# Performance work log

Measured on AMD Instinct MI355X. Metric: run time of the kernel, lower is better.

Reference implementation:

```python
import jax, jax.numpy as jnp
import numpy as np

EPS = 1e-5


def _lstm_agg(x, nbr_idx, Wih, Whh, bih, bhh):
    # x: [N, D] node feats; nbr_idx: [N, K]; LSTM hidden size == D (DGL lstm aggregator)
    seq = x[nbr_idx]                     # [N, K, D] irregular gather
    N, K, D = seq.shape
    seq_t = jnp.swapaxes(seq, 0, 1)      # [K, N, D] time-major for scan

    def step(carry, xt):
        h, c = carry
        z = xt @ Wih.T + bih + h @ Whh.T + bhh   # [N, 4D]; torch gate order i,f,g,o
        i, f, g, o = jnp.split(z, 4, axis=-1)
        i = jax.nn.sigmoid(i)
        f = jax.nn.sigmoid(f)
        g = jnp.tanh(g)
        o = jax.nn.sigmoid(o)
        c = f * c + i * g
        h = o * jnp.tanh(c)
        return (h, c), None

    zero = jnp.zeros((N, D), seq.dtype)
    (h, _), _ = jax.lax.scan(step, (zero, zero), seq_t)
    return h                             # final hidden state = neighbor aggregate


def _sage_layer(x, nbr_idx, Wih, Whh, bih, bhh, Wself, bself, Wneigh):
    h_neigh = _lstm_agg(x, nbr_idx, Wih, Whh, bih, bhh)
    return x @ Wself.T + bself + h_neigh @ Wneigh.T


def _bn(x, gamma, beta):
    # BatchNorm1d in training mode: batch statistics over the node axis
    mu = jnp.mean(x, axis=0)
    var = jnp.var(x, axis=0)
    return (x - mu) * jax.lax.rsqrt(var + EPS) * gamma + beta


def setup_inputs() -> dict:
    key = jax.random.key(0)
    N, K, D_IN, D_H = 100000, 16, 128, 128
    ks = jax.random.split(key, 20)
    s = 0.05
    inp = {
        "in_feat": jax.random.normal(ks[0], (N, D_IN), jnp.float32),
        "nbr_idx": jax.random.randint(ks[1], (N, K), 0, N, jnp.int32),
        # layer 1 (in_feats=128 -> h_feats=128), LSTM hidden = in_feats
        "Wih1": jax.random.normal(ks[2], (4 * D_IN, D_IN), jnp.float32) * s,
        "Whh1": jax.random.normal(ks[3], (4 * D_IN, D_IN), jnp.float32) * s,
        "bih1": jnp.zeros((4 * D_IN,), jnp.float32),
        "bhh1": jnp.zeros((4 * D_IN,), jnp.float32),
        "Wself1": jax.random.normal(ks[4], (D_H, D_IN), jnp.float32) * s,
        "bself1": jnp.zeros((D_H,), jnp.float32),
        "Wneigh1": jax.random.normal(ks[5], (D_H, D_IN), jnp.float32) * s,
        "gamma1": jnp.ones((D_H,), jnp.float32),
        "beta1": jnp.zeros((D_H,), jnp.float32),
        # layer 2 (h_feats=128 -> h_feats=128)
        "Wih2": jax.random.normal(ks[6], (4 * D_H, D_H), jnp.float32) * s,
        "Whh2": jax.random.normal(ks[7], (4 * D_H, D_H), jnp.float32) * s,
        "bih2": jnp.zeros((4 * D_H,), jnp.float32),
        "bhh2": jnp.zeros((4 * D_H,), jnp.float32),
        "Wself2": jax.random.normal(ks[8], (D_H, D_H), jnp.float32) * s,
        "bself2": jnp.zeros((D_H,), jnp.float32),
        "Wneigh2": jax.random.normal(ks[9], (D_H, D_H), jnp.float32) * s,
        "gamma2": jnp.ones((D_H,), jnp.float32),
        "beta2": jnp.zeros((D_H,), jnp.float32),
    }
    return inp


def reference(in_feat, nbr_idx,
              Wih1, Whh1, bih1, bhh1, Wself1, bself1, Wneigh1, gamma1, beta1,
              Wih2, Whh2, bih2, bhh2, Wself2, bself2, Wneigh2, gamma2, beta2):
    h = _sage_layer(in_feat, nbr_idx, Wih1, Whh1, bih1, bhh1, Wself1, bself1, Wneigh1)
    h = jax.nn.relu(_bn(h, gamma1, beta1))
    h = _sage_layer(h, nbr_idx, Wih2, Whh2, bih2, bhh2, Wself2, bself2, Wneigh2)
    h = _bn(h, gamma2, beta2)
    return h
```

## Files before the change

### kernel.cpp

```cpp
#include <hip/hip_runtime.h>

typedef unsigned short u16;
typedef unsigned int u32;
typedef unsigned long long u64;
typedef __attribute__((ext_vector_type(8))) short short8;
typedef __attribute__((ext_vector_type(4))) float float4_t;
typedef __attribute__((ext_vector_type(2))) u32 u32x2;

__device__ __forceinline__ u16 f2bf(float f) {
    union { float f; u32 u; } x; x.f = f;
    u32 r = x.u + 0x7FFFu + ((x.u >> 16) & 1u);
    return (u16)(r >> 16);
}
__device__ __forceinline__ float bitsf(u32 u) {
    union { u32 u; float f; } x; x.u = u; return x.f;
}
__device__ __forceinline__ u32 pk2bf(float hi, float lo) {
    union { float f; u32 u; } a, b; a.f = hi; b.f = lo;
    return __builtin_amdgcn_perm(a.u + 0x8000u, b.u + 0x8000u, 0x07060302u);
}
#define LOG2E 1.44269504088896340736f
__device__ __forceinline__ float tanh_(float x) {
    float t = __builtin_amdgcn_exp2f(2.f * LOG2E * x);
    return 1.f - 2.f * __builtin_amdgcn_rcpf(1.f + t);
}

__device__ __forceinline__ float4_t mfma16(short8 a, short8 b, float4_t c) {
    return __builtin_amdgcn_mfma_f32_16x16x32_bf16(a, b, c, 0, 0, 0);
}

#define LDS_BARRIER() asm volatile("s_waitcnt lgkmcnt(0)\n\ts_barrier" ::: "memory")

__device__ __forceinline__ short8 ldfrag(const u16* p) { return *(const short8*)p; }
__device__ __forceinline__ short8 ldfrag(const float* p) {
    float4_t a = *(const float4_t*)p;
    float4_t b = *(const float4_t*)(p + 4);
    short8 r;
#pragma unroll
    for (int j = 0; j < 4; ++j) { r[j] = (short)f2bf(a[j]); r[4 + j] = (short)f2bf(b[j]); }
    return r;
}
__device__ __forceinline__ short8 ldfrag_scaled(const float* p, float s) {
    float4_t a = *(const float4_t*)p;
    float4_t b = *(const float4_t*)(p + 4);
    short8 r;
#pragma unroll
    for (int j = 0; j < 4; ++j) { r[j] = (short)f2bf(a[j] * s); r[4 + j] = (short)f2bf(b[j] * s); }
    return r;
}

template<typename AT>
__global__ __launch_bounds__(256) void gemm_ih(
    const AT* __restrict__ A, const float* __restrict__ W,
    const float* __restrict__ b1, const float* __restrict__ b2,
    u16* __restrict__ C, float* __restrict__ stats, int M)
{
    if (blockIdx.x == 0 && blockIdx.y == 0) stats[threadIdx.x] = 0.f;
    const int P = 512;
    const int lane = threadIdx.x & 63;
    const int w    = threadIdx.x >> 6;
    const int l15  = lane & 15;
    const int quad = lane >> 4;
    const int rowbase = blockIdx.x * 64;
    const int colbase = blockIdx.y * 128 + w * 32;

    short8 af[4][4];
#pragma unroll
    for (int mb = 0; mb < 4; ++mb) {
        int row = rowbase + mb * 16 + l15;
        if (row >= M) row = M - 1;
        const AT* ap = A + (size_t)row * 128 + quad * 8;
#pragma unroll
        for (int kb = 0; kb < 4; ++kb) af[mb][kb] = ldfrag(ap + kb * 32);
    }
    short8 bfr[2][4];
#pragma unroll
    for (int nb = 0; nb < 2; ++nb) {
        int col = colbase + nb * 16 + l15;
        const float* wp = W + (size_t)col * 128 + quad * 8;
#pragma unroll
        for (int kb = 0; kb < 4; ++kb) bfr[nb][kb] = ldfrag(wp + kb * 32);
    }
    const float4_t z4 = {0.f, 0.f, 0.f, 0.f};
    float bias[2], scl[2];
#pragma unroll
    for (int nb = 0; nb < 2; ++nb) {
        int col = colbase + nb * 16 + l15;
        bias[nb] = b1[col] + b2[col];
        scl[nb] = (col >= 256 && col < 384) ? (2.f * LOG2E) : (-LOG2E);
    }
#pragma unroll
    for (int mb = 0; mb < 4; ++mb)
#pragma unroll
        for (int nb = 0; nb < 2; ++nb) {
            float4_t a = z4;
#pragma unroll
            for (int kb = 0; kb < 4; ++kb) a = mfma16(af[mb][kb], bfr[nb][kb], a);
#pragma unroll
            for (int r = 0; r < 4; ++r) {
                int row = rowbase + mb * 16 + quad * 4 + r;
                int col = colbase + nb * 16 + l15;
                if (row < M) C[(size_t)row * P + col] = f2bf((a[r] + bias[nb]) * scl[nb]);
            }
        }
}

template<typename T>
__device__ __forceinline__ void accum_gemm(
    const T* __restrict__ A, const float* __restrict__ W,
    float4_t (&acc)[4][2], int M, int rowbase, int colbase, int l15, int quad)
{
    short8 af[4][4];
#pragma unroll
    for (int mb = 0; mb < 4; ++mb) {
        int row = rowbase + mb * 16 + l15;
        if (row >= M) row = M - 1;
        const T* ap = A + (size_t)row * 128 + quad * 8;
#pragma unroll
        for (int kb = 0; kb < 4; ++kb) af[mb][kb] = ldfrag(ap + kb * 32);
    }
    short8 bfr[2][4];
#pragma unroll
    for (int nb = 0; nb < 2; ++nb) {
        int col = colbase + nb * 16 + l15;
        const float* wp = W + (size_t)col * 128 + quad * 8;
#pragma unroll
        for (int kb = 0; kb < 4; ++kb) bfr[nb][kb] = ldfrag(wp + kb * 32);
    }
#pragma unroll
    for (int mb = 0; mb < 4; ++mb)
#pragma unroll
        for (int nb = 0; nb < 2; ++nb)
#pragma unroll
            for (int kb = 0; kb < 4; ++kb)
                acc[mb][nb] = mfma16(af[mb][kb], bfr[nb][kb], acc[mb][nb]);
}

template<typename AT2>
__global__ __launch_bounds__(256) void gemm_out(
    const u16* __restrict__ A1, const float* __restrict__ W1,
    const AT2* __restrict__ A2, const float* __restrict__ W2,
    const float* __restrict__ bias, float* __restrict__ C,
    float* __restrict__ stats, int M)
{
    const int P = 128;
    const int lane = threadIdx.x & 63;
    const int w    = threadIdx.x >> 6;
    const int l15  = lane & 15;
    const int quad = lane >> 4;
    const int rowbase = blockIdx.x * 64;
    const int colbase = w * 32;

    float4_t acc[4][2];
    const float4_t z4 = {0.f, 0.f, 0.f, 0.f};
#pragma unroll
    for (int mb = 0; mb < 4; ++mb)
#pragma unroll
        for (int nb = 0; nb < 2; ++nb) acc[mb][nb] = z4;

    accum_gemm(A1, W1, acc, M, rowbase, colbase, l15, quad);
    accum_gemm(A2, W2, acc, M, rowbase, colbase, l15, quad);

    float s[2] = {0.f, 0.f}, sq[2] = {0.f, 0.f};
#pragma unroll
    for (int nb = 0; nb < 2; ++nb) {
        int col = colbase + nb * 16 + l15;
        float bb = bias[col];
#pragma unroll
        for (int mb = 0; mb < 4; ++mb)
#pragma unroll
            for (int r = 0; r < 4; ++r) {
                int row = rowbase + mb * 16 + quad * 4 + r;
                if (row < M) {
                    float v = acc[mb][nb][r] + bb;
                    C[(size_t)row * P + col] = v;
                    s[nb] += v; sq[nb] += v * v;
                }
            }
    }
#pragma unroll
    for (int nb = 0; nb < 2; ++nb) {
        float t1 = s[nb], t2 = sq[nb];
        t1 += __shfl_xor(t1, 16); t1 += __shfl_xor(t1, 32);
        t2 += __shfl_xor(t2, 16); t2 += __shfl_xor(t2, 32);
        int col = colbase + nb * 16 + l15;
        if (quad == 0) atomicAdd(&stats[col], t1);
        if (quad == 1) atomicAdd(&stats[P + col], t2);
    }
}

__global__ __launch_bounds__(512, 2) void lstm_kernel(
    const u16* __restrict__ Xih,
    const int* __restrict__ nbr,
    const float* __restrict__ Whh,
    u16* __restrict__ Hout,
    int N)
{
    __shared__ u16 hbuf[2][64][128];
    __shared__ int nbrs[16][72];
    const int tid  = threadIdx.x;
    const int lane = tid & 63;
    const int w    = tid >> 6;
    const int l15  = lane & 15;
    const int quad = lane >> 4;
    const int base = blockIdx.x * 64;

    short8 whA[4][4];
#pragma unroll
    for (int g = 0; g < 4; ++g) {
        int row = 128 * g + 16 * w + l15;
        float s = (g == 2) ? (2.f * LOG2E) : (-LOG2E);
        const float* wp = Whh + (size_t)row * 128 + quad * 8;
#pragma unroll
        for (int kb = 0; kb < 4; ++kb) whA[g][kb] = ldfrag_scaled(wp + kb * 32, s);
    }
    u32* hz = (u32*)&hbuf[0][0][0];
    for (int i = tid; i < 2 * 64 * 128 / 2; i += 512) hz[i] = 0u;
    for (int i = tid; i < 64 * 16; i += 512) {
        int node = base + (i >> 4);
        if (node >= N) node = N - 1;
        nbrs[i & 15][i >> 4] = nbr[(size_t)node * 16 + (i & 15)];
    }
    __syncthreads();

    const int xoff = 16 * w + 4 * quad;

    u32x2 xfu[4][4];
#pragma unroll
    for (int nb = 0; nb < 4; ++nb) {
        int node = nbrs[0][l15 + 16 * nb];
        const u16* xp = Xih + (size_t)node * 512 + xoff;
#pragma unroll
        for (int g = 0; g < 4; ++g) xfu[nb][g] = *(const u32x2*)(xp + 128 * g);
    }

    const float4_t z4 = {0.f, 0.f, 0.f, 0.f};
    float4_t c[4];
#pragma unroll
    for (int nb = 0; nb < 4; ++nb) c[nb] = z4;

    for (int t = 0; t < 16; ++t) {
        const int p = t & 1;
#pragma unroll
        for (int nb = 0; nb < 4; ++nb) {
            const int row = l15 + 16 * nb;
            float4_t z[4];
#pragma unroll
            for (int g = 0; g < 4; ++g) {
                u32 w0 = xfu[nb][g][0], w1 = xfu[nb][g][1];
                z[g][0] = bitsf(w0 << 16); z[g][1] = bitsf(w0 & 0xFFFF0000u);
                z[g][2] = bitsf(w1 << 16); z[g][3] = bitsf(w1 & 0xFFFF0000u);
            }
            if (t < 15) {
                int node = nbrs[t + 1][row];
                const u16* xp = Xih + (size_t)node * 512 + xoff;
#pragma unroll
                for (int g = 0; g < 4; ++g) xfu[nb][g] = *(const u32x2*)(xp + 128 * g);
            }
            const char* hrow = (const char*)&hbuf[p][row][0];
            __builtin_amdgcn_s_setprio(1);
#pragma unroll
            for (int kb = 0; kb < 4; ++kb) {
                int ch = (quad + 4 * kb) ^ (row & 7);
                short8 hb = *(const short8*)(hrow + (ch << 4));
#pragma unroll
                for (int g = 0; g < 4; ++g)
                    z[g] = mfma16(whA[g][kb], hb, z[g]);
            }
            __builtin_amdgcn_s_setprio(0);
            float4_t hv;
#pragma unroll
            for (int r = 0; r < 4; ++r) {
                float i_ = __builtin_amdgcn_rcpf(1.f + __builtin_amdgcn_exp2f(z[0][r]));
                float f_ = __builtin_amdgcn_rcpf(1.f + __builtin_amdgcn_exp2f(z[1][r]));
                float g_ = 1.f - 2.f * __builtin_amdgcn_rcpf(1.f + __builtin_amdgcn_exp2f(z[2][r]));
                float o_ = __builtin_amdgcn_rcpf(1.f + __builtin_amdgcn_exp2f(z[3][r]));
                float cc = f_ * c[nb][r] + i_ * g_;
                c[nb][r] = cc;
                hv[r] = o_ * tanh_(cc);
            }
            u64 pkd = ((u64)pk2bf(hv[3], hv[2]) << 32) | pk2bf(hv[1], hv[0]);
            if (t < 15) {
                int ch = (2 * w + (quad >> 1)) ^ (row & 7);
                int sw = (ch << 4) | ((quad & 1) << 3);
                *(u64*)((char*)&hbuf[1 - p][row][0] + sw) = pkd;
            } else {
                int grow = base + row;
                if (grow < N)
                    *(u64*)(Hout + (size_t)grow * 128 + xoff) = pkd;
            }
        }
        if (t < 15) LDS_BARRIER();
    }
}

__global__ void bn_prep(float* stats, const float* __restrict__ gamma,
                        const float* __restrict__ beta, float invN)
{
    int cidx = threadIdx.x;
    float s = stats[cidx], sq = stats[128 + cidx];
    float mu = s * invN;
    float var = sq * invN - mu * mu;
    float sc = gamma[cidx] * rsqrtf(var + 1e-5f);
    stats[256 + cidx] = sc;
    stats[384 + cidx] = beta[cidx] - mu * sc;
}

template<typename OT>
__global__ __launch_bounds__(256) void bn_apply(
    const float* __restrict__ X, const float* __restrict__ stats,
    OT* __restrict__ Y, int M, int relu)
{
    int gid = blockIdx.x * 256 + threadIdx.x;
    int row = gid >> 4;
    int cs  = (gid & 15) * 8;
    if (row >= M) return;
    float4_t a = *(const float4_t*)(X + (size_t)row * 128 + cs);
    float4_t b = *(const float4_t*)(X + (size_t)row * 128 + cs + 4);
    float v[8];
#pragma unroll
    for (int j = 0; j < 8; ++j) {
        float x = (j < 4) ? a[j] : b[j - 4];
        float t = x * stats[256 + cs + j] + stats[384 + cs + j];
        v[j] = relu ? fmaxf(t, 0.f) : t;
    }
    if constexpr (sizeof(OT) == 2) {
        short8 ov;
#pragma unroll
        for (int j = 0; j < 8; ++j) ov[j] = (short)f2bf(v[j]);
        *(short8*)((u16*)Y + (size_t)row * 128 + cs) = ov;
    } else {
        float4_t o1, o2;
#pragma unroll
        for (int j = 0; j < 4; ++j) { o1[j] = v[j]; o2[j] = v[4 + j]; }
        *(float4_t*)((float*)Y + (size_t)row * 128 + cs) = o1;
        *(float4_t*)((float*)Y + (size_t)row * 128 + cs + 4) = o2;
    }
}

extern "C" void kernel_launch(void* const* d_in, const int* in_sizes, int n_in,
                              void* d_out, int out_size, void* d_ws, size_t ws_size,
                              hipStream_t stream)
{
    const float* in_feat = (const float*)d_in[0];
    const int*   nbr     = (const int*)d_in[1];
    const float* Wih1 = (const float*)d_in[2];
    const float* Whh1 = (const float*)d_in[3];
    const float* bih1 = (const float*)d_in[4];
    const float* bhh1 = (const float*)d_in[5];
    const float* Wself1  = (const float*)d_in[6];
    const float* bself1  = (const float*)d_in[7];
    const float* Wneigh1 = (const float*)d_in[8];
    const float* gamma1  = (const float*)d_in[9];
    const float* beta1   = (const float*)d_in[10];
    const float* Wih2 = (const float*)d_in[11];
    const float* Whh2 = (const float*)d_in[12];
    const float* bih2 = (const float*)d_in[13];
    const float* bhh2 = (const float*)d_in[14];
    const float* Wself2  = (const float*)d_in[15];
    const float* bself2  = (const float*)d_in[16];
    const float* Wneigh2 = (const float*)d_in[17];
    const float* gamma2  = (const float*)d_in[18];
    const float* beta2   = (const float*)d_in[19];

    const int N = in_sizes[0] / 128;

    char* ws = (char*)d_ws;
    u16*   Xih   = (u16*)ws;
    float* Pbuf  = (float*)ws;
    u16*   hn    = (u16*)(ws + (size_t)N * 1024);
    float* stats = (float*)(ws + (size_t)N * 1024 + (size_t)N * 256);
    u16*   hcur  = (u16*)d_out;

    const int nblk = (N + 63) / 64;
    const float invN = 1.0f / (float)N;
    const int bnblk = (N * 16 + 255) / 256;

    gemm_ih<float><<<dim3(nblk, 4), dim3(256), 0, stream>>>(in_feat, Wih1, bih1, bhh1, Xih, stats, N);
    lstm_kernel<<<dim3(nblk), dim3(512), 0, stream>>>(Xih, nbr, Whh1, hn, N);
    gemm_out<float><<<dim3(nblk, 1), dim3(256), 0, stream>>>(hn, Wneigh1, in_feat, Wself1,
                                                             bself1, Pbuf, stats, N);
    bn_prep<<<dim3(1), dim3(128), 0, stream>>>(stats, gamma1, beta1, invN);
    bn_apply<u16><<<dim3(bnblk), dim3(256), 0, stream>>>(Pbuf, stats, hcur, N, 1);

    gemm_ih<u16><<<dim3(nblk, 4), dim3(256), 0, stream>>>(hcur, Wih2, bih2, bhh2, Xih, stats, N);
    lstm_kernel<<<dim3(nblk), dim3(512), 0, stream>>>(Xih, nbr, Whh2, hn, N);
    gemm_out<u16><<<dim3(nblk, 1), dim3(256), 0, stream>>>(hn, Wneigh2, hcur, Wself2,
                                                           bself2, Pbuf, stats, N);
    bn_prep<<<dim3(1), dim3(128), 0, stream>>>(stats, gamma2, beta2, invN);
    bn_apply<float><<<dim3(bnblk), dim3(256), 0, stream>>>(Pbuf, stats, (float*)d_out, N, 0);
}
```

Before: 1.538 ms.

## Restructure LSTM kernel so each wave owns nodes and keeps Whh in LDS

New measurement: 5.234 ms. 3.4x slower.

```diff
diff --git a/kernel.cpp b/kernel.cpp
--- a/kernel.cpp
+++ b/kernel.cpp
@@ -6,6 +6,7 @@
 typedef __attribute__((ext_vector_type(8))) short short8;
 typedef __attribute__((ext_vector_type(4))) float float4_t;
 typedef __attribute__((ext_vector_type(2))) u32 u32x2;
+typedef __attribute__((ext_vector_type(4))) u32 u32x4;
 
 __device__ __forceinline__ u16 f2bf(float f) {
     union { float f; u32 u; } x; x.f = f;
@@ -28,8 +29,6 @@
 __device__ __forceinline__ float4_t mfma16(short8 a, short8 b, float4_t c) {
     return __builtin_amdgcn_mfma_f32_16x16x32_bf16(a, b, c, 0, 0, 0);
 }
-
-#define LDS_BARRIER() asm volatile("s_waitcnt lgkmcnt(0)\n\ts_barrier" ::: "memory")
 
 __device__ __forceinline__ short8 ldfrag(const u16* p) { return *(const short8*)p; }
 __device__ __forceinline__ short8 ldfrag(const float* p) {
@@ -38,14 +37,6 @@
     short8 r;
 #pragma unroll
     for (int j = 0; j < 4; ++j) { r[j] = (short)f2bf(a[j]); r[4 + j] = (short)f2bf(b[j]); }
-    return r;
-}
-__device__ __forceinline__ short8 ldfrag_scaled(const float* p, float s) {
-    float4_t a = *(const float4_t*)p;
-    float4_t b = *(const float4_t*)(p + 4);
-    short8 r;
-#pragma unroll
-    for (int j = 0; j < 4; ++j) { r[j] = (short)f2bf(a[j] * s); r[4 + j] = (short)f2bf(b[j] * s); }
     return r;
 }
 
@@ -189,108 +180,138 @@
     }
 }
 
-__global__ __launch_bounds__(512, 2) void lstm_kernel(
+__global__ __launch_bounds__(512) void lstm_kernel(
     const u16* __restrict__ Xih,
     const int* __restrict__ nbr,
     const float* __restrict__ Whh,
     u16* __restrict__ Hout,
     int N)
 {
-    __shared__ u16 hbuf[2][64][128];
-    __shared__ int nbrs[16][72];
+    __shared__ u16 whs[512 * 128];
+    __shared__ u32 scr[8][32][16];
     const int tid  = threadIdx.x;
     const int lane = tid & 63;
     const int w    = tid >> 6;
     const int l15  = lane & 15;
     const int quad = lane >> 4;
-    const int base = blockIdx.x * 64;
-
-    short8 whA[4][4];
-#pragma unroll
-    for (int g = 0; g < 4; ++g) {
-        int row = 128 * g + 16 * w + l15;
-        float s = (g == 2) ? (2.f * LOG2E) : (-LOG2E);
-        const float* wp = Whh + (size_t)row * 128 + quad * 8;
-#pragma unroll
-        for (int kb = 0; kb < 4; ++kb) whA[g][kb] = ldfrag_scaled(wp + kb * 32, s);
-    }
-    u32* hz = (u32*)&hbuf[0][0][0];
-    for (int i = tid; i < 2 * 64 * 128 / 2; i += 512) hz[i] = 0u;
-    for (int i = tid; i < 64 * 16; i += 512) {
-        int node = base + (i >> 4);
-        if (node >= N) node = N - 1;
-        nbrs[i & 15][i >> 4] = nbr[(size_t)node * 16 + (i & 15)];
+    const int base = blockIdx.x * 256;
+
+    for (int i = tid; i < 512 * 16; i += 512) {
+        const int R = i >> 4, cch = i & 15;
+        const float s = ((R >> 7) == 2) ? (2.f * LOG2E) : (-LOG2E);
+        const float* wp = Whh + (size_t)R * 128 + cch * 8;
+        float4_t a = *(const float4_t*)wp;
+        float4_t b = *(const float4_t*)(wp + 4);
+        u32x4 pk;
+        pk[0] = ((u32)f2bf(a[1] * s) << 16) | f2bf(a[0] * s);
+        pk[1] = ((u32)f2bf(a[3] * s) << 16) | f2bf(a[2] * s);
+        pk[2] = ((u32)f2bf(b[1] * s) << 16) | f2bf(b[0] * s);
+        pk[3] = ((u32)f2bf(b[3] * s) << 16) | f2bf(b[2] * s);
+        *(u32x4*)&whs[R * 128 + ((cch ^ (R & 15)) << 3)] = pk;
     }
     __syncthreads();
 
-    const int xoff = 16 * w + 4 * quad;
-
-    u32x2 xfu[4][4];
-#pragma unroll
-    for (int nb = 0; nb < 4; ++nb) {
-        int node = nbrs[0][l15 + 16 * nb];
-        const u16* xp = Xih + (size_t)node * 512 + xoff;
-#pragma unroll
-        for (int g = 0; g < 4; ++g) xfu[nb][g] = *(const u32x2*)(xp + 128 * g);
-    }
+    const int own0s = base + w * 32 + l15;
+    const int own1s = own0s + 16;
+    const int own0 = own0s < N ? own0s : N - 1;
+    const int own1 = own1s < N ? own1s : N - 1;
+
+    int xcur0 = nbr[(size_t)own0 * 16];
+    int xcur1 = nbr[(size_t)own1 * 16];
 
     const float4_t z4 = {0.f, 0.f, 0.f, 0.f};
-    float4_t c[4];
-#pragma unroll
-    for (int nb = 0; nb < 4; ++nb) c[nb] = z4;
+    float4_t c[8][2];
+#pragma unroll
+    for (int dc = 0; dc < 8; ++dc) { c[dc][0] = z4; c[dc][1] = z4; }
+    const short8 zs8 = {0, 0, 0, 0, 0, 0, 0, 0};
+    short8 hfA[2][4];
+#pragma unroll
+    for (int n = 0; n < 2; ++n)
+#pragma unroll
+        for (int kb = 0; kb < 4; ++kb) hfA[n][kb] = zs8;
 
     for (int t = 0; t < 16; ++t) {
-        const int p = t & 1;
-#pragma unroll
-        for (int nb = 0; nb < 4; ++nb) {
-            const int row = l15 + 16 * nb;
-            float4_t z[4];
-#pragma unroll
-            for (int g = 0; g < 4; ++g) {
-                u32 w0 = xfu[nb][g][0], w1 = xfu[nb][g][1];
-                z[g][0] = bitsf(w0 << 16); z[g][1] = bitsf(w0 & 0xFFFF0000u);
-                z[g][2] = bitsf(w1 << 16); z[g][3] = bitsf(w1 & 0xFFFF0000u);
+        int xn0 = 0, xn1 = 0;
+        if (t < 15) {
+            xn0 = nbr[(size_t)own0 * 16 + t + 1];
+            xn1 = nbr[(size_t)own1 * 16 + t + 1];
+        }
+        const u16* bp0 = Xih + (size_t)xcur0 * 512 + 4 * quad;
+        const u16* bp1 = Xih + (size_t)xcur1 * 512 + 4 * quad;
+
+        u32x2 gb[2][2][4];
+#pragma unroll
+        for (int g = 0; g < 4; ++g) {
+            gb[0][0][g] = *(const u32x2*)(bp0 + 128 * g);
+            gb[0][1][g] = *(const u32x2*)(bp1 + 128 * g);
+        }
+        short8 hfB[2][4];
+#pragma unroll
+        for (int dc = 0; dc < 8; ++dc) {
+            const int par = dc & 1;
+            if (dc < 7) {
+#pragma unroll
+                for (int g = 0; g < 4; ++g) {
+                    gb[par ^ 1][0][g] = *(const u32x2*)(bp0 + 128 * g + 16 * (dc + 1));
+                    gb[par ^ 1][1][g] = *(const u32x2*)(bp1 + 128 * g + 16 * (dc + 1));
+                }
             }
-            if (t < 15) {
-                int node = nbrs[t + 1][row];
-                const u16* xp = Xih + (size_t)node * 512 + xoff;
-#pragma unroll
-                for (int g = 0; g < 4; ++g) xfu[nb][g] = *(const u32x2*)(xp + 128 * g);
+            float4_t z[4][2];
+#pragma unroll
+            for (int g = 0; g < 4; ++g)
+#pragma unroll
+                for (int n = 0; n < 2; ++n) {
+                    u32 w0 = gb[par][n][g][0], w1 = gb[par][n][g][1];
+                    z[g][n][0] = bitsf(w0 << 16); z[g][n][1] = bitsf(w0 & 0xFFFF0000u);
+                    z[g][n][2] = bitsf(w1 << 16); z[g][n][3] = bitsf(w1 & 0xFFFF0000u);
+                }
+#pragma unroll
+            for (int kb = 0; kb < 4; ++kb)
+#pragma unroll
+                for (int g = 0; g < 4; ++g) {
+                    const short8 whf = *(const short8*)&whs[
+                        (128 * g + 16 * dc + l15) * 128 +
+                        ((((kb << 2) | quad) ^ l15) << 3)];
+                    z[g][0] = mfma16(whf, hfA[0][kb], z[g][0]);
+                    z[g][1] = mfma16(whf, hfA[1][kb], z[g][1]);
+                }
+#pragma unroll
+            for (int n = 0; n < 2; ++n) {
+                float4_t hv;
+#pragma unroll
+                for (int r = 0; r < 4; ++r) {
+                    float i_ = __builtin_amdgcn_rcpf(1.f + __builtin_amdgcn_exp2f(z[0][n][r]));
+                    float f_ = __builtin_amdgcn_rcpf(1.f + __builtin_amdgcn_exp2f(z[1][n][r]));
+                    float g_ = 1.f - 2.f * __builtin_amdgcn_rcpf(1.f + __builtin_amdgcn_exp2f(z[2][n][r]));
+                    float o_ = __builtin_amdgcn_rcpf(1.f + __builtin_amdgcn_exp2f(z[3][n][r]));
+                    float cc = f_ * c[dc][n][r] + i_ * g_;
+                    c[dc][n][r] = cc;
+                    hv[r] = o_ * tanh_(cc);
+                }
+                u32x2 pr;
+                pr[0] = pk2bf(hv[1], hv[0]);
+                pr[1] = pk2bf(hv[3], hv[2]);
+                if (t < 15) {
+                    *(u32x2*)&scr[w][n * 16 + l15][8 * par + 2 * quad] = pr;
+                } else {
+                    const int own = n ? own1s : own0s;
+                    if (own < N)
+                        *(u32x2*)(Hout + (size_t)own * 128 + 16 * dc + 4 * quad) = pr;
+                }
             }
-            const char* hrow = (const char*)&hbuf[p][row][0];
-            __builtin_amdgcn_s_setprio(1);
-#pragma unroll
-            for (int kb = 0; kb < 4; ++kb) {
-                int ch = (quad + 4 * kb) ^ (row & 7);
-                short8 hb = *(const short8*)(hrow + (ch << 4));
-#pragma unroll
-                for (int g = 0; g < 4; ++g)
-                    z[g] = mfma16(whA[g][kb], hb, z[g]);
-            }
-            __builtin_amdgcn_s_setprio(0);
-            float4_t hv;
-#pragma unroll
-            for (int r = 0; r < 4; ++r) {
-                float i_ = __builtin_amdgcn_rcpf(1.f + __builtin_amdgcn_exp2f(z[0][r]));
-                float f_ = __builtin_amdgcn_rcpf(1.f + __builtin_amdgcn_exp2f(z[1][r]));
-                float g_ = 1.f - 2.f * __builtin_amdgcn_rcpf(1.f + __builtin_amdgcn_exp2f(z[2][r]));
-                float o_ = __builtin_amdgcn_rcpf(1.f + __builtin_amdgcn_exp2f(z[3][r]));
-                float cc = f_ * c[nb][r] + i_ * g_;
-                c[nb][r] = cc;
-                hv[r] = o_ * tanh_(cc);
-            }
-            u64 pkd = ((u64)pk2bf(hv[3], hv[2]) << 32) | pk2bf(hv[1], hv[0]);
-            if (t < 15) {
-                int ch = (2 * w + (quad >> 1)) ^ (row & 7);
-                int sw = (ch << 4) | ((quad & 1) << 3);
-                *(u64*)((char*)&hbuf[1 - p][row][0] + sw) = pkd;
-            } else {
-                int grow = base + row;
-                if (grow < N)
-                    *(u64*)(Hout + (size_t)grow * 128 + xoff) = pkd;
+            if (par && t < 15) {
+                const int kb = dc >> 1;
+                hfB[0][kb] = *(const short8*)&scr[w][l15][4 * quad];
+                hfB[1][kb] = *(const short8*)&scr[w][16 + l15][4 * quad];
             }
         }
-        if (t < 15) LDS_BARRIER();
+        if (t < 15) {
+#pragma unroll
+            for (int n = 0; n < 2; ++n)
+#pragma unroll
+                for (int kb = 0; kb < 4; ++kb) hfA[n][kb] = hfB[n][kb];
+            xcur0 = xn0; xcur1 = xn1;
+        }
     }
 }
 
@@ -373,18 +394,19 @@
     u16*   hcur  = (u16*)d_out;
 
     const int nblk = (N + 63) / 64;
+    const int lblk = (N + 255) / 256;
     const float invN = 1.0f / (float)N;
     const int bnblk = (N * 16 + 255) / 256;
 
     gemm_ih<float><<<dim3(nblk, 4), dim3(256), 0, stream>>>(in_feat, Wih1, bih1, bhh1, Xih, stats, N);
-    lstm_kernel<<<dim3(nblk), dim3(512), 0, stream>>>(Xih, nbr, Whh1, hn, N);
+    lstm_kernel<<<dim3(lblk), dim3(512), 0, stream>>>(Xih, nbr, Whh1, hn, N);
     gemm_out<float><<<dim3(nblk, 1), dim3(256), 0, stream>>>(hn, Wneigh1, in_feat, Wself1,
                                                              bself1, Pbuf, stats, N);
     bn_prep<<<dim3(1), dim3(128), 0, stream>>>(stats, gamma1, beta1, invN);
     bn_apply<u16><<<dim3(bnblk), dim3(256), 0, stream>>>(Pbuf, stats, hcur, N, 1);
 
     gemm_ih<u16><<<dim3(nblk, 4), dim3(256), 0, stream>>>(hcur, Wih2, bih2, bhh2, Xih, stats, N);
-    lstm_kernel<<<dim3(nblk), dim3(512), 0, stream>>>(Xih, nbr, Whh2, hn, N);
+    lstm_kernel<<<dim3(lblk), dim3(512), 0, stream>>>(Xih, nbr, Whh2, hn, N);
     gemm_out<u16><<<dim3(nblk, 1), dim3(256), 0, stream>>>(hn, Wneigh2, hcur, Wself2,
                                                            bself2, Pbuf, stats, N);
     bn_prep<<<dim3(1), dim3(128), 0, stream>>>(stats, gamma2, beta2, invN);
```
